# Kernel optimization log

Hardware: AMD Instinct MI355X
Metric: run time of the kernel (lower is better)

The kernel has to match this reference:

```python
import jax, jax.numpy as jnp
import numpy as np

EPS = 1e-8
N = 1024          # number of points
C = 16            # channels per layer
RBF_LOW, RBF_HIGH, RBF_COUNT = 0.0, 3.5, 32


def _rand(key, shape, scale=0.1):
    return scale * jax.random.normal(key, shape, dtype=jnp.float32)


def setup_inputs() -> dict:
    key = jax.random.key(0)
    ks = jax.random.split(key, 20)
    R = RBF_COUNT
    return {
        'points':   jax.random.normal(ks[0], (N, 3), dtype=jnp.float32),
        # layer 1: 2 radial filters (0->0 and 0->1), output_dim = 1 input channel
        'l1_W1':    _rand(ks[1],  (2, R, R)),
        'l1_B1':    _rand(ks[2],  (2, R)),
        'l1_W2':    _rand(ks[3],  (2, R, 1)),
        'l1_B2':    _rand(ks[4],  (2, 1)),
        'l1_si0_w': _rand(ks[5],  (C, 1)),
        'l1_si0_b': _rand(ks[6],  (C,)),
        'l1_si1_w': _rand(ks[7],  (C, 1)),
        'l1_nl_b':  _rand(ks[8],  (C,)),
        # layer 2: 5 radial filters (0->0, 0->1, 1->0, 1->1 id, 1->1 levi-civita)
        'l2_W1':    _rand(ks[9],  (5, R, R)),
        'l2_B1':    _rand(ks[10], (5, R)),
        'l2_W2':    _rand(ks[11], (5, R, C)),
        'l2_B2':    _rand(ks[12], (5, C)),
        'l2_si0_w': _rand(ks[13], (C, 2 * C)),
        'l2_si0_b': _rand(ks[14], (C,)),
        'l2_si1_w': _rand(ks[15], (C, 3 * C)),
        'l2_nl_b':  _rand(ks[16], (C,)),
        # readout
        'fc_w':     _rand(ks[17], (C, 8)),
        'fc_b':     _rand(ks[18], (8,)),
    }


def _eijk():
    e = np.zeros((3, 3, 3), dtype=np.float32)
    e[0, 1, 2] = e[1, 2, 0] = e[2, 0, 1] = 1.0
    e[0, 2, 1] = e[2, 1, 0] = e[1, 0, 2] = -1.0
    return jnp.asarray(e)


def _norm_eps(x, axis, keepdims=False):
    # norm_with_epsilon: sqrt(max(sum(x^2), EPS))
    return jnp.sqrt(jnp.maximum(jnp.sum(x * x, axis=axis, keepdims=keepdims), EPS))


def _radial(rbf, w1, b1, w2, b2):
    # R(): two-layer relu MLP on rbf features -> [N, N, F]
    h = jax.nn.relu(rbf @ w1 + b1)
    return h @ w2 + b2


def _geometry(points):
    rij = points[:, None, :] - points[None, :, :]          # [N,N,3]
    ss = jnp.sum(rij * rij, axis=-1)                        # [N,N]
    mask0 = ss < EPS                                        # dij == 0 (diagonal)
    dij = jnp.where(mask0, 0.0, jnp.sqrt(jnp.where(mask0, 1.0, ss)))
    centers = jnp.linspace(RBF_LOW, RBF_HIGH, RBF_COUNT, dtype=jnp.float32)
    gamma = jnp.float32(RBF_COUNT / (RBF_HIGH - RBF_LOW))
    rbf = jnp.exp(-gamma * (dij[..., None] - centers) ** 2)  # [N,N,RBF]
    unit = rij / _norm_eps(rij, axis=-1, keepdims=True)       # unit_vectors
    return rbf, unit, mask0


def _F1(rad, unit, mask0):
    # F_1: mask radial where dij==0, multiply by unit vectors -> [N,N,F,3]
    mr = jnp.where(mask0[..., None], 0.0, rad)
    return mr[..., None] * unit[:, :, None, :]


def _nonlinearity(x0, x1, b1):
    # degree-0: pointwise elu; degree-1: norm nonlinearity x * elu(|x|+b)/|x|
    x0 = jax.nn.elu(x0)
    n = _norm_eps(x1, axis=-1)                              # [N,C]
    x1 = x1 * (jax.nn.elu(n + b1) / n)[..., None]
    return x0, x1


def reference(points, l1_W1, l1_B1, l1_W2, l1_B2, l1_si0_w, l1_si0_b, l1_si1_w,
              l1_nl_b, l2_W1, l2_B1, l2_W2, l2_B2, l2_si0_w, l2_si0_b, l2_si1_w,
              l2_nl_b, fc_w, fc_b):
    rbf, unit, mask0 = _geometry(points)
    eijk = _eijk().astype(points.dtype)
    n_pts = points.shape[0]
    x0 = jnp.ones((n_pts, 1, 1), dtype=points.dtype)        # degree-0 input [N,1,1]

    # ---- layer 1: only degree-0 input -> (0->0) and (0->1) filters ----
    r00 = _radial(rbf, l1_W1[0], l1_B1[0], l1_W2[0], l1_B2[0])
    out0 = jnp.einsum('abf,bfi->afi', r00, x0)              # filter_0
    F1a = _F1(_radial(rbf, l1_W1[1], l1_B1[1], l1_W2[1], l1_B2[1]), unit, mask0)
    out1 = jnp.einsum('abfi,bf->afi', F1a, x0[..., 0])
    x0 = jnp.einsum('afi,gf->agi', out0, l1_si0_w) + l1_si0_b[:, None]
    x1 = jnp.einsum('afi,gf->agi', out1, l1_si1_w)
    x0, x1 = _nonlinearity(x0, x1, l1_nl_b)                 # [N,C,1], [N,C,3]

    # ---- layer 2: degree-0 and degree-1 inputs -> 5 filters ----
    rads = [_radial(rbf, l2_W1[i], l2_B1[i], l2_W2[i], l2_B2[i]) for i in range(5)]
    c00 = jnp.einsum('abf,bfi->afi', rads[0], x0)                          # 0x0->0
    c01 = jnp.einsum('abfi,bf->afi', _F1(rads[1], unit, mask0), x0[..., 0])  # 0x1->1
    c10 = jnp.einsum('abfj,bfj->af', _F1(rads[2], unit, mask0), x1)[..., None]  # 1x1->0
    c11 = jnp.einsum('abf,bfi->afi', rads[3], x1)                          # 1x0->1
    c11x = jnp.einsum('ijk,abfj,bfk->afi', eijk, _F1(rads[4], unit, mask0), x1)  # 1x1->1
    cat0 = jnp.concatenate([c00, c10], axis=-2)             # [N,2C,1]
    cat1 = jnp.concatenate([c01, c11, c11x], axis=-2)       # [N,3C,3]
    x0 = jnp.einsum('afi,gf->agi', cat0, l2_si0_w) + l2_si0_b[:, None]
    x1 = jnp.einsum('afi,gf->agi', cat1, l2_si1_w)
    x0, x1 = _nonlinearity(x0, x1, l2_nl_b)

    # ---- readout: invariant degree-0 features, mean-pool over points ----
    g = jnp.mean(x0[..., 0], axis=0)                        # [C]
    return g @ fc_w + fc_b                                  # [num_classes]
```

## Files before the change

kernel.cpp:

```cpp
#include <hip/hip_runtime.h>
#include <hip/hip_bf16.h>
#include <math.h>

#define NP 1024
#define R 32
#define C 16
#define GAMMA (32.0f/3.5f)
#define DC (3.5f/31.0f)
#define NBANK 32

typedef __attribute__((ext_vector_type(8))) short bf16x8;
typedef __attribute__((ext_vector_type(4))) float f32x4;

__device__ __forceinline__ short tobf(float x){
    __hip_bfloat16 h = __float2bfloat16(x);
    return __builtin_bit_cast(short, h);
}
__device__ __forceinline__ float frombf(short s){
    __hip_bfloat16 h = __builtin_bit_cast(__hip_bfloat16, s);
    return __bfloat162float(h);
}
__device__ __forceinline__ unsigned pack2bf(float a, float b){
    const unsigned lo = (unsigned short)tobf(a);
    const unsigned hi = (unsigned short)tobf(b);
    return lo | (hi << 16);
}
__device__ __forceinline__ float eluf(float x){ return x > 0.f ? x : expm1f(x); }

__device__ __forceinline__ f32x4 mfma16(bf16x8 a, bf16x8 b, f32x4 c){
    return __builtin_amdgcn_mfma_f32_16x16x32_bf16(a, b, c, 0, 0, 0);
}

template<int STRIDE>
__device__ __forceinline__ void load_bfrag(const float* __restrict__ src, int q, int n,
                                           bf16x8& hi, bf16x8& lo){
    #pragma unroll
    for (int jj = 0; jj < 8; jj++){
        const float w = src[(q*8+jj)*STRIDE + n];
        const short h = tobf(w);
        hi[jj] = h;
        lo[jj] = tobf(w - frombf(h));
    }
}

__global__ __launch_bounds__(256) void k_l1p(
    const float* __restrict__ points,
    const float* __restrict__ W1, const float* __restrict__ B1,
    const float* __restrict__ W2, const float* __restrict__ B2,
    const float* __restrict__ si0w, const float* __restrict__ si0b,
    const float* __restrict__ si1w, const float* __restrict__ nlb,
    float* __restrict__ x0g, float* __restrict__ x1s,
    float* __restrict__ partial, unsigned* __restrict__ cnt)
{
    __shared__ float sS0[4][32];
    __shared__ float sT[4][32][3];
    __shared__ float sUp[4][3];
    __shared__ float sO[4];

    const int tid  = threadIdx.x;
    const int lane = tid & 63;
    const int wv   = tid >> 6;
    const int l16  = lane & 15;
    const int q    = lane >> 4;
    const int a    = blockIdx.x;
    const float pax = points[a*3+0], pay = points[a*3+1], paz = points[a*3+2];

    bf16x8 w1hi[2][2], w1lo[2][2];
    float  b1v[2][2];
    #pragma unroll
    for (int fi = 0; fi < 2; fi++)
        #pragma unroll
        for (int nt = 0; nt < 2; nt++){
            load_bfrag<R>(W1 + fi*R*R, q, nt*16 + l16, w1hi[fi][nt], w1lo[fi][nt]);
            b1v[fi][nt] = B1[fi*R + nt*16 + l16];
        }

    float s0a[2] = {0.f, 0.f};
    float T[2][3] = {};
    float upx = 0.f, upy = 0.f, upz = 0.f;

    for (int bt = 0; bt < 16; bt++){
        const int bA = bt*64 + wv*16 + l16;
        const float rx = pax - points[bA*3+0];
        const float ry = pay - points[bA*3+1];
        const float rz = paz - points[bA*3+2];
        const float ss = rx*rx + ry*ry + rz*rz;
        const float dij = sqrtf(ss);
        const float inv = 1.0f / sqrtf(fmaxf(ss, 1e-8f));
        const float ux = rx*inv, uy = ry*inv, uz = rz*inv;
        upx += ux; upy += uy; upz += uz;

        bf16x8 afrag;
        #pragma unroll
        for (int jj = 0; jj < 8; jj++){
            const float t = dij - (float)(q*8+jj)*DC;
            afrag[jj] = tobf(__expf(-GAMMA*t*t));
        }

        float uxr[4], uyr[4], uzr[4];
        #pragma unroll
        for (int r4 = 0; r4 < 4; r4++){
            const int sl = q*4 + r4;
            uxr[r4] = __shfl(ux, sl, 16);
            uyr[r4] = __shfl(uy, sl, 16);
            uzr[r4] = __shfl(uz, sl, 16);
        }

        #pragma unroll
        for (int nt = 0; nt < 2; nt++){
            f32x4 c = {b1v[0][nt], b1v[0][nt], b1v[0][nt], b1v[0][nt]};
            c = mfma16(afrag, w1hi[0][nt], c);
            c = mfma16(afrag, w1lo[0][nt], c);
            s0a[nt] += fmaxf(c[0],0.f)+fmaxf(c[1],0.f)+fmaxf(c[2],0.f)+fmaxf(c[3],0.f);
        }
        #pragma unroll
        for (int nt = 0; nt < 2; nt++){
            f32x4 c = {b1v[1][nt], b1v[1][nt], b1v[1][nt], b1v[1][nt]};
            c = mfma16(afrag, w1hi[1][nt], c);
            c = mfma16(afrag, w1lo[1][nt], c);
            #pragma unroll
            for (int r4 = 0; r4 < 4; r4++){
                const float h = fmaxf(c[r4], 0.f);
                T[nt][0] = fmaf(h, uxr[r4], T[nt][0]);
                T[nt][1] = fmaf(h, uyr[r4], T[nt][1]);
                T[nt][2] = fmaf(h, uzr[r4], T[nt][2]);
            }
        }
    }

    #pragma unroll
    for (int nt = 0; nt < 2; nt++){
        s0a[nt] += __shfl_down(s0a[nt], 32, 64);
        s0a[nt] += __shfl_down(s0a[nt], 16, 64);
        #pragma unroll
        for (int i = 0; i < 3; i++){
            T[nt][i] += __shfl_down(T[nt][i], 32, 64);
            T[nt][i] += __shfl_down(T[nt][i], 16, 64);
        }
    }
    #pragma unroll
    for (int off = 32; off > 0; off >>= 1){
        upx += __shfl_down(upx, off, 64);
        upy += __shfl_down(upy, off, 64);
        upz += __shfl_down(upz, off, 64);
    }
    if (lane < 16){
        sS0[wv][lane]      = s0a[0];
        sS0[wv][16 + lane] = s0a[1];
        #pragma unroll
        for (int i = 0; i < 3; i++){
            sT[wv][lane][i]      = T[0][i];
            sT[wv][16 + lane][i] = T[1][i];
        }
    }
    if (lane == 0){ sUp[wv][0] = upx; sUp[wv][1] = upy; sUp[wv][2] = upz; }
    __syncthreads();
    if (tid == 0){
        float o0 = 0.f;
        for (int j = 0; j < R; j++){
            const float S = sS0[0][j] + sS0[1][j] + sS0[2][j] + sS0[3][j];
            o0 = fmaf(S, W2[j], o0);
        }
        sO[0] = o0 + (float)NP * B2[0];
        for (int i = 0; i < 3; i++){
            float t = 0.f;
            for (int j = 0; j < R; j++){
                const float Tj = sT[0][j][i] + sT[1][j][i] + sT[2][j][i] + sT[3][j][i];
                t = fmaf(Tj, W2[R + j], t);
            }
            const float Ui = 0.25f * (sUp[0][i] + sUp[1][i] + sUp[2][i] + sUp[3][i]);
            sO[1+i] = t + B2[1] * Ui;
        }
    }
    __syncthreads();
    if (tid < C){
        const int g = tid;
        const float o0 = sO[0];
        const float o1x = sO[1], o1y = sO[2], o1z = sO[3];
        x0g[a*C+g] = eluf(fmaf(o0, si0w[g], si0b[g]));
        const float w = si1w[g];
        const float tx = o1x*w, ty = o1y*w, tz = o1z*w;
        const float n = sqrtf(fmaxf(tx*tx + ty*ty + tz*tz, 1e-8f));
        const float sc = eluf(n + nlb[g]) / n;
        x1s[0*NP*C + a*C+g] = tx*sc;
        x1s[1*NP*C + a*C+g] = ty*sc;
        x1s[2*NP*C + a*C+g] = tz*sc;
    }
    if (a == 0){
        partial[tid]       = 0.f;
        partial[256 + tid] = 0.f;
        if (tid < NBANK) cnt[tid] = __float_as_uint(0.f) * 0u;
        if (tid < NBANK) ((unsigned*)cnt)[tid] = 0u;
        if (tid == 0) ((unsigned*)cnt)[NBANK] = 0u;
    }
}

__global__ __launch_bounds__(256) void k_l2r(
    const float* __restrict__ points,
    const float* __restrict__ W1, const float* __restrict__ B1,
    const float* __restrict__ W2, const float* __restrict__ B2,
    const float* __restrict__ x0g, const float* __restrict__ x1s,
    const float* __restrict__ si0w, const float* __restrict__ si0b,
    const float* __restrict__ fcw, const float* __restrict__ fcb,
    float* __restrict__ partial, unsigned* __restrict__ cnt,
    float* __restrict__ out)
{
    __shared__ __align__(16) short sH[4][2][16*40];
    __shared__ float sRed[4][2][16];
    __shared__ float sC[2][16];
    __shared__ float sP[16];
    __shared__ unsigned amLast;

    const int tid  = threadIdx.x;
    const int lane = tid & 63;
    const int wv   = tid >> 6;
    const int l16  = lane & 15;
    const int q    = lane >> 4;
    const int a    = blockIdx.x;
    const float pax = points[a*3+0], pay = points[a*3+1], paz = points[a*3+2];

    bf16x8 w1hi[2][2], w1lo[2][2], w2hi[2], w2lo[2];
    float  b1v[2][2], b2v[2];
    #pragma unroll
    for (int fi = 0; fi < 2; fi++){
        const int fx = (fi == 0) ? 0 : 2;
        #pragma unroll
        for (int nt = 0; nt < 2; nt++){
            load_bfrag<R>(W1 + fx*R*R, q, 2*l16 + nt, w1hi[fi][nt], w1lo[fi][nt]);
            b1v[fi][nt] = B1[fx*R + 2*l16 + nt];
        }
        load_bfrag<C>(W2 + fx*R*C, q, l16, w2hi[fi], w2lo[fi]);
        b2v[fi] = B2[fx*C + l16];
    }

    float acc0 = 0.f, acc1 = 0.f;
    short* sH0 = sH[wv][0];
    short* sH1 = sH[wv][1];

    for (int bt = 0; bt < 16; bt++){
        const int bA = bt*64 + wv*16 + l16;
        const float rx = pax - points[bA*3+0];
        const float ry = pay - points[bA*3+1];
        const float rz = paz - points[bA*3+2];
        const float ss = rx*rx + ry*ry + rz*rz;
        const float dij = sqrtf(ss);
        const float inv = 1.0f / sqrtf(fmaxf(ss, 1e-8f));
        const float ux = rx*inv, uy = ry*inv, uz = rz*inv;

        float uxr[4], uyr[4], uzr[4];
        #pragma unroll
        for (int r4 = 0; r4 < 4; r4++){
            const int sl = q*4 + r4;
            uxr[r4] = __shfl(ux, sl, 16);
            uyr[r4] = __shfl(uy, sl, 16);
            uzr[r4] = __shfl(uz, sl, 16);
        }

        const int rb = (bt*64 + wv*16 + q*4)*C + l16;
        float x0v[4], udv[4];
        #pragma unroll
        for (int r4 = 0; r4 < 4; r4++){
            x0v[r4] = x0g[rb + r4*C];
            const float v0 = x1s[0*NP*C + rb + r4*C];
            const float v1 = x1s[1*NP*C + rb + r4*C];
            const float v2 = x1s[2*NP*C + rb + r4*C];
            udv[r4] = uxr[r4]*v0 + uyr[r4]*v1 + uzr[r4]*v2;
        }

        bf16x8 afrag;
        #pragma unroll
        for (int jj = 0; jj < 8; jj++){
            const float t = dij - (float)(q*8+jj)*DC;
            afrag[jj] = tobf(__expf(-GAMMA*t*t));
        }

        #pragma unroll
        for (int fi = 0; fi < 2; fi++){
            f32x4 c0 = {b1v[fi][0], b1v[fi][0], b1v[fi][0], b1v[fi][0]};
            c0 = mfma16(afrag, w1hi[fi][0], c0);
            c0 = mfma16(afrag, w1lo[fi][0], c0);
            f32x4 c1 = {b1v[fi][1], b1v[fi][1], b1v[fi][1], b1v[fi][1]};
            c1 = mfma16(afrag, w1hi[fi][1], c1);
            c1 = mfma16(afrag, w1lo[fi][1], c1);
            short* sHf = (fi == 0) ? sH0 : sH1;
            #pragma unroll
            for (int r4 = 0; r4 < 4; r4++){
                const unsigned p = pack2bf(fmaxf(c0[r4], 0.f), fmaxf(c1[r4], 0.f));
                *(unsigned*)&sHf[(q*4+r4)*40 + 2*l16] = p;
            }
        }
        asm volatile("s_waitcnt lgkmcnt(0)" ::: "memory");
        #pragma unroll
        for (int fi = 0; fi < 2; fi++){
            const short* sHf = (fi == 0) ? sH0 : sH1;
            const bf16x8 hf = *(const bf16x8*)(sHf + l16*40 + q*8);
            f32x4 d = {0.f, 0.f, 0.f, 0.f};
            d = mfma16(hf, w2hi[fi], d);
            d = mfma16(hf, w2lo[fi], d);
            #pragma unroll
            for (int r4 = 0; r4 < 4; r4++){
                const float v = d[r4] + b2v[fi];
                if (fi == 0) acc0 = fmaf(v, x0v[r4], acc0);
                else         acc1 = fmaf(v, udv[r4], acc1);
            }
        }
    }

    acc0 += __shfl_down(acc0, 32, 64); acc0 += __shfl_down(acc0, 16, 64);
    acc1 += __shfl_down(acc1, 32, 64); acc1 += __shfl_down(acc1, 16, 64);
    if (lane < 16){ sRed[wv][0][lane] = acc0; sRed[wv][1][lane] = acc1; }
    __syncthreads();
    if (tid < 16){
        sC[0][tid] = sRed[0][0][tid] + sRed[1][0][tid] + sRed[2][0][tid] + sRed[3][0][tid];
        sC[1][tid] = sRed[0][1][tid] + sRed[1][1][tid] + sRed[2][1][tid] + sRed[3][1][tid];
    }
    __syncthreads();
    if (tid < C){
        const int g = tid;
        float s = si0b[g];
        #pragma unroll
        for (int f = 0; f < C; f++) s = fmaf(sC[0][f], si0w[g*2*C + f], s);
        #pragma unroll
        for (int f = 0; f < C; f++) s = fmaf(sC[1][f], si0w[g*2*C + C + f], s);
        atomicAdd(&partial[(a & (NBANK-1))*C + g], eluf(s));
    }
    __syncthreads();
    if (tid == 0){
        amLast = 0u;
        const unsigned p1 = atomicAdd(&cnt[a & (NBANK-1)], 1u);
        if (p1 == (NP/NBANK) - 1u){
            const unsigned p2 = atomicAdd(&cnt[NBANK], 1u);
            if (p2 == NBANK - 1u) amLast = 1u;
        }
    }
    __syncthreads();
    if (amLast){
        if (tid < C){
            float v = 0.f;
            #pragma unroll
            for (int b = 0; b < NBANK; b++)
                v += __hip_atomic_load(&partial[b*C + tid], __ATOMIC_RELAXED,
                                       __HIP_MEMORY_SCOPE_AGENT);
            sP[tid] = v;
        }
        __syncthreads();
        if (tid < 8){
            float s = fcb[tid];
            #pragma unroll
            for (int g = 0; g < C; g++)
                s = fmaf(sP[g] * (1.0f / (float)NP), fcw[g*8 + tid], s);
            out[tid] = s;
        }
    }
}

extern "C" void kernel_launch(void* const* d_in, const int* in_sizes, int n_in,
                              void* d_out, int out_size, void* d_ws, size_t ws_size,
                              hipStream_t stream)
{
    (void)in_sizes; (void)n_in; (void)out_size; (void)ws_size;
    const float* points   = (const float*)d_in[0];
    const float* l1_W1    = (const float*)d_in[1];
    const float* l1_B1    = (const float*)d_in[2];
    const float* l1_W2    = (const float*)d_in[3];
    const float* l1_B2    = (const float*)d_in[4];
    const float* l1_si0_w = (const float*)d_in[5];
    const float* l1_si0_b = (const float*)d_in[6];
    const float* l1_si1_w = (const float*)d_in[7];
    const float* l1_nl_b  = (const float*)d_in[8];
    const float* l2_W1    = (const float*)d_in[9];
    const float* l2_B1    = (const float*)d_in[10];
    const float* l2_W2    = (const float*)d_in[11];
    const float* l2_B2    = (const float*)d_in[12];
    const float* l2_si0_w = (const float*)d_in[13];
    const float* l2_si0_b = (const float*)d_in[14];
    const float* fc_w     = (const float*)d_in[17];
    const float* fc_b     = (const float*)d_in[18];

    float* ws       = (float*)d_ws;
    float* x0g      = ws;
    float* x1s      = x0g + NP*C;
    float* partial  = x1s + 3*NP*C;
    unsigned* cnt   = (unsigned*)(partial + NBANK*C);

    k_l1p<<<NP, 256, 0, stream>>>(points, l1_W1, l1_B1, l1_W2, l1_B2,
                                  l1_si0_w, l1_si0_b, l1_si1_w, l1_nl_b,
                                  x0g, x1s, partial, cnt);
    k_l2r<<<NP, 256, 0, stream>>>(points, l2_W1, l2_B1, l2_W2, l2_B2,
                                  x0g, x1s, l2_si0_w, l2_si0_b,
                                  fc_w, fc_b, partial, cnt, (float*)d_out);
}
```

Measured before the change: 160.5 us.

## Drop split-bf16 MFMA compensation and split layer-2 rows across two blocks

The hi/lo bf16 split of the weights is removed, so every radial MLP matmul issues one MFMA instead of two. Layer 2 now launches two blocks per point, each covering half of the neighbour range. Partial c00/c10 sums are combined with global atomics and a per-point counter, and the second block to finish does the self-interaction and readout. Launch bounds now ask for 8 blocks per CU. This halves MFMA work and doubles parallelism, but lowers weight precision to plain bf16 and adds atomic traffic and extra workspace.

```diff
diff --git a/kernel.cpp b/kernel.cpp
--- a/kernel.cpp
+++ b/kernel.cpp
@@ -16,10 +16,6 @@
     __hip_bfloat16 h = __float2bfloat16(x);
     return __builtin_bit_cast(short, h);
 }
-__device__ __forceinline__ float frombf(short s){
-    __hip_bfloat16 h = __builtin_bit_cast(__hip_bfloat16, s);
-    return __bfloat162float(h);
-}
 __device__ __forceinline__ unsigned pack2bf(float a, float b){
     const unsigned lo = (unsigned short)tobf(a);
     const unsigned hi = (unsigned short)tobf(b);
@@ -33,14 +29,10 @@
 
 template<int STRIDE>
 __device__ __forceinline__ void load_bfrag(const float* __restrict__ src, int q, int n,
-                                           bf16x8& hi, bf16x8& lo){
+                                           bf16x8& w){
     #pragma unroll
-    for (int jj = 0; jj < 8; jj++){
-        const float w = src[(q*8+jj)*STRIDE + n];
-        const short h = tobf(w);
-        hi[jj] = h;
-        lo[jj] = tobf(w - frombf(h));
-    }
+    for (int jj = 0; jj < 8; jj++)
+        w[jj] = tobf(src[(q*8+jj)*STRIDE + n]);
 }
 
 __global__ __launch_bounds__(256) void k_l1p(
@@ -50,6 +42,8 @@
     const float* __restrict__ si0w, const float* __restrict__ si0b,
     const float* __restrict__ si1w, const float* __restrict__ nlb,
     float* __restrict__ x0g, float* __restrict__ x1s,
+    float* __restrict__ c00g, float* __restrict__ c10g,
+    unsigned* __restrict__ cntA,
     float* __restrict__ partial, unsigned* __restrict__ cnt)
 {
     __shared__ float sS0[4][32];
@@ -65,13 +59,13 @@
     const int a    = blockIdx.x;
     const float pax = points[a*3+0], pay = points[a*3+1], paz = points[a*3+2];
 
-    bf16x8 w1hi[2][2], w1lo[2][2];
+    bf16x8 w1f[2][2];
     float  b1v[2][2];
     #pragma unroll
     for (int fi = 0; fi < 2; fi++)
         #pragma unroll
         for (int nt = 0; nt < 2; nt++){
-            load_bfrag<R>(W1 + fi*R*R, q, nt*16 + l16, w1hi[fi][nt], w1lo[fi][nt]);
+            load_bfrag<R>(W1 + fi*R*R, q, nt*16 + l16, w1f[fi][nt]);
             b1v[fi][nt] = B1[fi*R + nt*16 + l16];
         }
 
@@ -109,15 +103,13 @@
         #pragma unroll
         for (int nt = 0; nt < 2; nt++){
             f32x4 c = {b1v[0][nt], b1v[0][nt], b1v[0][nt], b1v[0][nt]};
-            c = mfma16(afrag, w1hi[0][nt], c);
-            c = mfma16(afrag, w1lo[0][nt], c);
+            c = mfma16(afrag, w1f[0][nt], c);
             s0a[nt] += fmaxf(c[0],0.f)+fmaxf(c[1],0.f)+fmaxf(c[2],0.f)+fmaxf(c[3],0.f);
         }
         #pragma unroll
         for (int nt = 0; nt < 2; nt++){
             f32x4 c = {b1v[1][nt], b1v[1][nt], b1v[1][nt], b1v[1][nt]};
-            c = mfma16(afrag, w1hi[1][nt], c);
-            c = mfma16(afrag, w1lo[1][nt], c);
+            c = mfma16(afrag, w1f[1][nt], c);
             #pragma unroll
             for (int r4 = 0; r4 < 4; r4++){
                 const float h = fmaxf(c[r4], 0.f);
@@ -186,50 +178,53 @@
         x1s[1*NP*C + a*C+g] = ty*sc;
         x1s[2*NP*C + a*C+g] = tz*sc;
     }
+    if (tid < C){ c00g[a*C + tid] = 0.f; c10g[a*C + tid] = 0.f; }
+    if (tid == 0) cntA[a] = 0u;
     if (a == 0){
         partial[tid]       = 0.f;
         partial[256 + tid] = 0.f;
-        if (tid < NBANK) cnt[tid] = __float_as_uint(0.f) * 0u;
-        if (tid < NBANK) ((unsigned*)cnt)[tid] = 0u;
-        if (tid == 0) ((unsigned*)cnt)[NBANK] = 0u;
-    }
-}
-
-__global__ __launch_bounds__(256) void k_l2r(
+        if (tid < NBANK) cnt[tid] = 0u;
+        if (tid == 0) cnt[NBANK] = 0u;
+    }
+}
+
+__global__ __launch_bounds__(256, 8) void k_l2r(
     const float* __restrict__ points,
     const float* __restrict__ W1, const float* __restrict__ B1,
     const float* __restrict__ W2, const float* __restrict__ B2,
     const float* __restrict__ x0g, const float* __restrict__ x1s,
     const float* __restrict__ si0w, const float* __restrict__ si0b,
     const float* __restrict__ fcw, const float* __restrict__ fcb,
+    float* __restrict__ c00g, float* __restrict__ c10g,
+    unsigned* __restrict__ cntA,
     float* __restrict__ partial, unsigned* __restrict__ cnt,
     float* __restrict__ out)
 {
     __shared__ __align__(16) short sH[4][2][16*40];
     __shared__ float sRed[4][2][16];
-    __shared__ float sC[2][16];
     __shared__ float sP[16];
-    __shared__ unsigned amLast;
+    __shared__ unsigned aDone, amLast;
 
     const int tid  = threadIdx.x;
     const int lane = tid & 63;
     const int wv   = tid >> 6;
     const int l16  = lane & 15;
     const int q    = lane >> 4;
-    const int a    = blockIdx.x;
+    const int a    = blockIdx.x >> 1;
+    const int half = blockIdx.x & 1;
     const float pax = points[a*3+0], pay = points[a*3+1], paz = points[a*3+2];
 
-    bf16x8 w1hi[2][2], w1lo[2][2], w2hi[2], w2lo[2];
+    bf16x8 w1f[2][2], w2f[2];
     float  b1v[2][2], b2v[2];
     #pragma unroll
     for (int fi = 0; fi < 2; fi++){
         const int fx = (fi == 0) ? 0 : 2;
         #pragma unroll
         for (int nt = 0; nt < 2; nt++){
-            load_bfrag<R>(W1 + fx*R*R, q, 2*l16 + nt, w1hi[fi][nt], w1lo[fi][nt]);
+            load_bfrag<R>(W1 + fx*R*R, q, 2*l16 + nt, w1f[fi][nt]);
             b1v[fi][nt] = B1[fx*R + 2*l16 + nt];
         }
-        load_bfrag<C>(W2 + fx*R*C, q, l16, w2hi[fi], w2lo[fi]);
+        load_bfrag<C>(W2 + fx*R*C, q, l16, w2f[fi]);
         b2v[fi] = B2[fx*C + l16];
     }
 
@@ -237,7 +232,7 @@
     short* sH0 = sH[wv][0];
     short* sH1 = sH[wv][1];
 
-    for (int bt = 0; bt < 16; bt++){
+    for (int bt = half*8; bt < half*8 + 8; bt++){
         const int bA = bt*64 + wv*16 + l16;
         const float rx = pax - points[bA*3+0];
         const float ry = pay - points[bA*3+1];
@@ -277,11 +272,9 @@
         #pragma unroll
         for (int fi = 0; fi < 2; fi++){
             f32x4 c0 = {b1v[fi][0], b1v[fi][0], b1v[fi][0], b1v[fi][0]};
-            c0 = mfma16(afrag, w1hi[fi][0], c0);
-            c0 = mfma16(afrag, w1lo[fi][0], c0);
+            c0 = mfma16(afrag, w1f[fi][0], c0);
             f32x4 c1 = {b1v[fi][1], b1v[fi][1], b1v[fi][1], b1v[fi][1]};
-            c1 = mfma16(afrag, w1hi[fi][1], c1);
-            c1 = mfma16(afrag, w1lo[fi][1], c1);
+            c1 = mfma16(afrag, w1f[fi][1], c1);
             short* sHf = (fi == 0) ? sH0 : sH1;
             #pragma unroll
             for (int r4 = 0; r4 < 4; r4++){
@@ -295,8 +288,7 @@
             const short* sHf = (fi == 0) ? sH0 : sH1;
             const bf16x8 hf = *(const bf16x8*)(sHf + l16*40 + q*8);
             f32x4 d = {0.f, 0.f, 0.f, 0.f};
-            d = mfma16(hf, w2hi[fi], d);
-            d = mfma16(hf, w2lo[fi], d);
+            d = mfma16(hf, w2f[fi], d);
             #pragma unroll
             for (int r4 = 0; r4 < 4; r4++){
                 const float v = d[r4] + b2v[fi];
@@ -310,46 +302,64 @@
     acc1 += __shfl_down(acc1, 32, 64); acc1 += __shfl_down(acc1, 16, 64);
     if (lane < 16){ sRed[wv][0][lane] = acc0; sRed[wv][1][lane] = acc1; }
     __syncthreads();
-    if (tid < 16){
-        sC[0][tid] = sRed[0][0][tid] + sRed[1][0][tid] + sRed[2][0][tid] + sRed[3][0][tid];
-        sC[1][tid] = sRed[0][1][tid] + sRed[1][1][tid] + sRed[2][1][tid] + sRed[3][1][tid];
+    if (tid < 16)
+        atomicAdd(&c00g[a*C + tid],
+                  sRed[0][0][tid] + sRed[1][0][tid] + sRed[2][0][tid] + sRed[3][0][tid]);
+    else if (tid < 32){
+        const int f = tid - 16;
+        atomicAdd(&c10g[a*C + f],
+                  sRed[0][1][f] + sRed[1][1][f] + sRed[2][1][f] + sRed[3][1][f]);
     }
     __syncthreads();
-    if (tid < C){
-        const int g = tid;
-        float s = si0b[g];
-        #pragma unroll
-        for (int f = 0; f < C; f++) s = fmaf(sC[0][f], si0w[g*2*C + f], s);
-        #pragma unroll
-        for (int f = 0; f < C; f++) s = fmaf(sC[1][f], si0w[g*2*C + C + f], s);
-        atomicAdd(&partial[(a & (NBANK-1))*C + g], eluf(s));
-    }
+    if (tid == 0)
+        aDone = (atomicAdd(&cntA[a], 1u) == 1u) ? 1u : 0u;
     __syncthreads();
-    if (tid == 0){
-        amLast = 0u;
-        const unsigned p1 = atomicAdd(&cnt[a & (NBANK-1)], 1u);
-        if (p1 == (NP/NBANK) - 1u){
-            const unsigned p2 = atomicAdd(&cnt[NBANK], 1u);
-            if (p2 == NBANK - 1u) amLast = 1u;
-        }
-    }
-    __syncthreads();
-    if (amLast){
+
+    if (aDone){
         if (tid < C){
-            float v = 0.f;
+            const int g = tid;
+            float s = si0b[g];
             #pragma unroll
-            for (int b = 0; b < NBANK; b++)
-                v += __hip_atomic_load(&partial[b*C + tid], __ATOMIC_RELAXED,
-                                       __HIP_MEMORY_SCOPE_AGENT);
-            sP[tid] = v;
+            for (int f = 0; f < C; f++){
+                const float v0 = __hip_atomic_load(&c00g[a*C + f], __ATOMIC_RELAXED,
+                                                   __HIP_MEMORY_SCOPE_AGENT);
+                s = fmaf(v0, si0w[g*2*C + f], s);
+            }
+            #pragma unroll
+            for (int f = 0; f < C; f++){
+                const float v1 = __hip_atomic_load(&c10g[a*C + f], __ATOMIC_RELAXED,
+                                                   __HIP_MEMORY_SCOPE_AGENT);
+                s = fmaf(v1, si0w[g*2*C + C + f], s);
+            }
+            atomicAdd(&partial[(a & (NBANK-1))*C + g], eluf(s));
         }
         __syncthreads();
-        if (tid < 8){
-            float s = fcb[tid];
-            #pragma unroll
-            for (int g = 0; g < C; g++)
-                s = fmaf(sP[g] * (1.0f / (float)NP), fcw[g*8 + tid], s);
-            out[tid] = s;
+        if (tid == 0){
+            amLast = 0u;
+            const unsigned p1 = atomicAdd(&cnt[a & (NBANK-1)], 1u);
+            if (p1 == (NP/NBANK) - 1u){
+                const unsigned p2 = atomicAdd(&cnt[NBANK], 1u);
+                if (p2 == NBANK - 1u) amLast = 1u;
+            }
+        }
+        __syncthreads();
+        if (amLast){
+            if (tid < C){
+                float v = 0.f;
+                #pragma unroll
+                for (int b = 0; b < NBANK; b++)
+                    v += __hip_atomic_load(&partial[b*C + tid], __ATOMIC_RELAXED,
+                                           __HIP_MEMORY_SCOPE_AGENT);
+                sP[tid] = v;
+            }
+            __syncthreads();
+            if (tid < 8){
+                float s = fcb[tid];
+                #pragma unroll
+                for (int g = 0; g < C; g++)
+                    s = fmaf(sP[g] * (1.0f / (float)NP), fcw[g*8 + tid], s);
+                out[tid] = s;
+            }
         }
     }
 }
@@ -380,13 +390,17 @@
     float* ws       = (float*)d_ws;
     float* x0g      = ws;
     float* x1s      = x0g + NP*C;
-    float* partial  = x1s + 3*NP*C;
+    float* c00g     = x1s + 3*NP*C;
+    float* c10g     = c00g + NP*C;
+    float* partial  = c10g + NP*C;
     unsigned* cnt   = (unsigned*)(partial + NBANK*C);
+    unsigned* cntA  = cnt + NBANK + 1;
 
     k_l1p<<<NP, 256, 0, stream>>>(points, l1_W1, l1_B1, l1_W2, l1_B2,
                                   l1_si0_w, l1_si0_b, l1_si1_w, l1_nl_b,
-                                  x0g, x1s, partial, cnt);
-    k_l2r<<<NP, 256, 0, stream>>>(points, l2_W1, l2_B1, l2_W2, l2_B2,
-                                  x0g, x1s, l2_si0_w, l2_si0_b,
-                                  fc_w, fc_b, partial, cnt, (float*)d_out);
-}
+                                  x0g, x1s, c00g, c10g, cntA, partial, cnt);
+    k_l2r<<<2*NP, 256, 0, stream>>>(points, l2_W1, l2_B1, l2_W2, l2_B2,
+                                    x0g, x1s, l2_si0_w, l2_si0_b,
+                                    fc_w, fc_b, c00g, c10g, cntA,
+                                    partial, cnt, (float*)d_out);
+}
```

Measured after the change: 219.4 us. 36.7% more time.
